# Optimization experiments

Hardware: AMD Instinct MI355X
Metric: run time of the kernel (lower is better)

## Reference

```python
import jax, jax.numpy as jnp
import numpy as np

N_NODES = 100000
N_EDGES = 1600000
IN_DIM = 256
OUT_DIM = 128
EPS = 1e-12  # torch F.normalize default eps


def setup_inputs() -> dict:
    key = jax.random.key(0)
    k1, k2, k3, k4, k5 = jax.random.split(key, 5)
    x = jax.random.normal(k1, (N_NODES, IN_DIM), dtype=jnp.float32)
    edge_index = jax.random.randint(k2, (2, N_EDGES), 0, N_NODES, dtype=jnp.int64)
    # projection (no bias): weight [out, in]
    Wp = jax.random.normal(k3, (OUT_DIM, IN_DIM), dtype=jnp.float32) * 0.05
    # GCNConv internal linear weight [out, out] and output bias [out]
    Wg = jax.random.normal(k4, (OUT_DIM, OUT_DIM), dtype=jnp.float32) * 0.05
    bg = jax.random.normal(k5, (OUT_DIM,), dtype=jnp.float32) * 0.01
    return {"x": x, "edge_index": edge_index, "Wp": Wp, "Wg": Wg, "bg": bg}


def reference(x, edge_index, Wp, Wg, bg):
    n = x.shape[0]
    # projection: x @ Wp^T
    h = x @ Wp.T                      # [N, OUT]
    # GCNConv: transform first, then propagate
    h = h @ Wg.T                      # [N, OUT]
    # add self-loops
    loops = jnp.arange(n, dtype=edge_index.dtype)
    row = jnp.concatenate([edge_index[0], loops])   # source
    col = jnp.concatenate([edge_index[1], loops])   # target
    # symmetric normalization: deg over target index (edge_weight = 1)
    deg = jax.ops.segment_sum(jnp.ones_like(col, dtype=h.dtype), col, num_segments=n)
    dinv = jnp.where(deg > 0, jax.lax.rsqrt(deg), 0.0)
    norm = dinv[row] * dinv[col]                     # [E+N]
    # gather messages from source, scale, scatter-add to target
    msg = h[row] * norm[:, None]                     # [E+N, OUT]
    out = jax.ops.segment_sum(msg, col, num_segments=n)  # [N, OUT]
    out = out + bg
    # F.normalize(dim=1): divide by L2 norm clamped at eps
    nrm = jnp.sqrt(jnp.sum(out * out, axis=1, keepdims=True))
    out = out / jnp.maximum(nrm, EPS)
    return out
```

## Files before the change

kernel.cpp:

```cpp
#include <hip/hip_runtime.h>
#include <hip/hip_fp16.h>

#define NDIM 128
#define KDIM 256
#define MT 5
#define AROW 264
#define CHUNK 6400
#define MAXBUCK 128

typedef _Float16 half8 __attribute__((ext_vector_type(8)));
typedef float float4v __attribute__((ext_vector_type(4)));

__global__ void k_combine_w(const float* __restrict__ Wp, const float* __restrict__ Wg,
                            _Float16* __restrict__ Bfrag) {
    int o = blockIdx.x;
    int i = threadIdx.x;
    float acc = 0.f;
#pragma unroll 4
    for (int k = 0; k < 128; ++k) acc = fmaf(Wg[o * 128 + k], Wp[k * 256 + i], acc);
    int kk = i >> 5, r = i & 31, quad = r >> 3, j = r & 7;
    int ntile = o >> 4, lanen = o & 15, lane = quad * 16 + lanen;
    Bfrag[(((ntile * 8 + kk) * 64) + lane) * 8 + j] = (_Float16)acc;
}

__global__ __launch_bounds__(256) void k_phase1(const int* __restrict__ col, int E,
                                                int* __restrict__ hist, int NBLK, int NBUCK) {
    __shared__ int h[MAXBUCK];
    int tid = threadIdx.x;
    if (tid < MAXBUCK) h[tid] = 0;
    __syncthreads();
    int e0 = blockIdx.x * CHUNK;
    int e1 = min(e0 + CHUNK, E);
    for (int e = e0 + tid; e < e1; e += 256) atomicAdd(&h[col[e] >> 10], 1);
    __syncthreads();
    if (tid < NBUCK) hist[tid * NBLK + blockIdx.x] = h[tid];
}

__global__ __launch_bounds__(1024) void k_scan2(int* __restrict__ hist, int NE) {
    __shared__ int s[1024];
    int t = threadIdx.x;
    int CH = (NE + 1023) >> 10;
    int off = t * CH;
    int sum = 0;
    for (int j = 0; j < CH; ++j) { int idx = off + j; if (idx < NE) sum += hist[idx]; }
    s[t] = sum;
    __syncthreads();
    for (int d = 1; d < 1024; d <<= 1) {
        int y = (t >= d) ? s[t - d] : 0;
        __syncthreads();
        s[t] += y;
        __syncthreads();
    }
    int run = s[t] - sum;
    for (int j = 0; j < CH; ++j) {
        int idx = off + j;
        if (idx < NE) { int v = hist[idx]; hist[idx] = run; run += v; }
    }
}

__global__ __launch_bounds__(256) void k_phase3(const int* __restrict__ ei, int E,
                                                const int* __restrict__ offs, int NBLK, int NBUCK,
                                                int2* __restrict__ tmp) {
    __shared__ int cur[MAXBUCK];
    int tid = threadIdx.x;
    if (tid < NBUCK) cur[tid] = offs[tid * NBLK + blockIdx.x];
    __syncthreads();
    int e0 = blockIdx.x * CHUNK;
    int e1 = min(e0 + CHUNK, E);
    for (int e = e0 + tid; e < e1; e += 256) {
        int r = ei[e];
        int c = ei[E + e];
        int p = atomicAdd(&cur[c >> 10], 1);
        tmp[p] = make_int2(r, c);
    }
}

__global__ __launch_bounds__(1024) void k_fine(const int2* __restrict__ tmp,
                                               const int* __restrict__ offs, int NBLK, int NBUCK,
                                               int N, int E,
                                               int* __restrict__ sortedRow,
                                               int* __restrict__ cnt,
                                               int* __restrict__ rowStart) {
    __shared__ int scnt[1024];
    __shared__ int cur[1024];
    int b = blockIdx.x;
    int t = threadIdx.x;
    int nodeBase = b << 10;
    int start = offs[b * NBLK];
    int end = (b + 1 < NBUCK) ? offs[(b + 1) * NBLK] : E;

    scnt[t] = 0;
    __syncthreads();
    for (int p = start + t; p < end; p += 1024) atomicAdd(&scnt[tmp[p].y - nodeBase], 1);
    __syncthreads();
    int v = scnt[t];
    for (int d = 1; d < 1024; d <<= 1) {
        int y = (t >= d) ? scnt[t - d] : 0;
        __syncthreads();
        scnt[t] += y;
        __syncthreads();
    }
    int excl = scnt[t] - v;
    int node = nodeBase + t;
    if (node < N) {
        cnt[node] = v;
        rowStart[node] = start + excl;
    }
    cur[t] = start + excl;
    __syncthreads();
    for (int p = start + t; p < end; p += 1024) {
        int2 pr = tmp[p];
        int slot = atomicAdd(&cur[pr.y - nodeBase], 1);
        sortedRow[slot] = pr.x;
    }
    if (b == NBUCK - 1 && t == 0) rowStart[N] = E;
}

__global__ __launch_bounds__(256) void k_gemm_mfma(const float* __restrict__ x,
                                                   const _Float16* __restrict__ Bfrag,
                                                   const int* __restrict__ cnt,
                                                   _Float16* __restrict__ g, int nrows) {
    __shared__ __align__(16) _Float16 xs[16 * AROW];
    int tid  = threadIdx.x;
    int lane = tid & 63;
    int w    = tid >> 6;
    int quad = lane >> 4;
    int lcol = lane & 15;

    const half8* Bv = (const half8*)Bfrag;
    half8 b0[8], b1[8];
#pragma unroll
    for (int kk = 0; kk < 8; ++kk) {
        b0[kk] = Bv[(w * 8 + kk) * 64 + lane];
        b1[kk] = Bv[((w + 4) * 8 + kk) * 64 + lane];
    }

    long base = (long)blockIdx.x * (16 * MT);
    for (int t = 0; t < MT; ++t) {
        long m0 = base + t * 16;
        __syncthreads();
        const float4* xv = (const float4*)(x + m0 * KDIM);
#pragma unroll
        for (int ii = 0; ii < 4; ++ii) {
            int idx = tid + ii * 256;
            int m = idx >> 6, k4 = idx & 63;
            float4 v = xv[idx];
            _Float16* d = &xs[m * AROW + k4 * 4];
            d[0] = (_Float16)v.x; d[1] = (_Float16)v.y;
            d[2] = (_Float16)v.z; d[3] = (_Float16)v.w;
        }
        __syncthreads();

        float4v acc0 = {0.f, 0.f, 0.f, 0.f}, acc1 = {0.f, 0.f, 0.f, 0.f};
#pragma unroll
        for (int kk = 0; kk < 8; ++kk) {
            half8 a = *(const half8*)(&xs[lcol * AROW + kk * 32 + quad * 8]);
            acc0 = __builtin_amdgcn_mfma_f32_16x16x32_f16(a, b0[kk], acc0, 0, 0, 0);
            acc1 = __builtin_amdgcn_mfma_f32_16x16x32_f16(a, b1[kk], acc1, 0, 0, 0);
        }

#pragma unroll
        for (int r = 0; r < 4; ++r) {
            long node = m0 + quad * 4 + r;
            float di = rsqrtf((float)(cnt[node] + 1));
            g[node * NDIM + w * 16 + lcol]        = (_Float16)(acc0[r] * di);
            g[node * NDIM + (w + 4) * 16 + lcol]  = (_Float16)(acc1[r] * di);
        }
    }
}

__global__ __launch_bounds__(256) void k_gather(const _Float16* __restrict__ g,
                                                const int* __restrict__ rowStart,
                                                const int* __restrict__ sortedRow,
                                                const int* __restrict__ cnt,
                                                const float* __restrict__ bg,
                                                float* __restrict__ out) {
    int lane = threadIdx.x & 63;
    int i = blockIdx.x * 4 + (threadIdx.x >> 6);
    const int s = rowStart[i];
    const int e = rowStart[i + 1];
    const int g4  = lane >> 4;
    const int r16 = lane & 15;

    const half8* __restrict__ gv = (const half8*)g;

    float acc[8];
#pragma unroll
    for (int j = 0; j < 8; ++j) acc[j] = 0.f;

    int p = s;
    for (; p + 16 <= e; p += 16) {
        int r0 = sortedRow[p + g4];
        int r1 = sortedRow[p + 4 + g4];
        int r2 = sortedRow[p + 8 + g4];
        int r3 = sortedRow[p + 12 + g4];
        half8 v0 = gv[(size_t)r0 * 16 + r16];
        half8 v1 = gv[(size_t)r1 * 16 + r16];
        half8 v2 = gv[(size_t)r2 * 16 + r16];
        half8 v3 = gv[(size_t)r3 * 16 + r16];
#pragma unroll
        for (int j = 0; j < 8; ++j)
            acc[j] += ((float)v0[j] + (float)v1[j]) + ((float)v2[j] + (float)v3[j]);
    }
    for (; p + 4 <= e; p += 4) {
        int r0 = sortedRow[p + g4];
        half8 v0 = gv[(size_t)r0 * 16 + r16];
#pragma unroll
        for (int j = 0; j < 8; ++j) acc[j] += (float)v0[j];
    }
    if (p + g4 < e) {
        int r0 = sortedRow[p + g4];
        half8 v0 = gv[(size_t)r0 * 16 + r16];
#pragma unroll
        for (int j = 0; j < 8; ++j) acc[j] += (float)v0[j];
    }

#pragma unroll
    for (int j = 0; j < 8; ++j) {
        acc[j] += __shfl_xor(acc[j], 16);
        acc[j] += __shfl_xor(acc[j], 32);
    }

    half8 sv = gv[(size_t)i * 16 + r16];
#pragma unroll
    for (int j = 0; j < 8; ++j) acc[j] += (float)sv[j];

    float di = rsqrtf((float)(cnt[i] + 1));
    float4 b0 = ((const float4*)bg)[r16 * 2];
    float4 b1 = ((const float4*)bg)[r16 * 2 + 1];
    float v[8];
    v[0] = fmaf(di, acc[0], b0.x);
    v[1] = fmaf(di, acc[1], b0.y);
    v[2] = fmaf(di, acc[2], b0.z);
    v[3] = fmaf(di, acc[3], b0.w);
    v[4] = fmaf(di, acc[4], b1.x);
    v[5] = fmaf(di, acc[5], b1.y);
    v[6] = fmaf(di, acc[6], b1.z);
    v[7] = fmaf(di, acc[7], b1.w);

    float sq = 0.f;
#pragma unroll
    for (int j = 0; j < 8; ++j) sq += v[j] * v[j];
    sq += __shfl_xor(sq, 1);
    sq += __shfl_xor(sq, 2);
    sq += __shfl_xor(sq, 4);
    sq += __shfl_xor(sq, 8);
    float scale = 1.0f / fmaxf(sqrtf(sq), 1e-12f);

    if (g4 == 0) {
        float4 o0 = make_float4(v[0] * scale, v[1] * scale, v[2] * scale, v[3] * scale);
        float4 o1 = make_float4(v[4] * scale, v[5] * scale, v[6] * scale, v[7] * scale);
        ((float4*)out)[(size_t)i * 32 + r16 * 2]     = o0;
        ((float4*)out)[(size_t)i * 32 + r16 * 2 + 1] = o1;
    }
}

extern "C" void kernel_launch(void* const* d_in, const int* in_sizes, int n_in,
                              void* d_out, int out_size, void* d_ws, size_t ws_size,
                              hipStream_t stream) {
    const float* x  = (const float*)d_in[0];
    const int*   ei = (const int*)  d_in[1];
    const float* Wp = (const float*)d_in[2];
    const float* Wg = (const float*)d_in[3];
    const float* bg = (const float*)d_in[4];
    float* out = (float*)d_out;

    const int N = in_sizes[0] / KDIM;
    const int E = in_sizes[1] / 2;

    const int NBLK  = (E + CHUNK - 1) / CHUNK;
    const int NBUCK = (N + 1023) >> 10;
    const int NE    = NBLK * NBUCK;

    char* p = (char*)d_ws;
    auto carve = [&](size_t bytes) { void* r = (void*)p; p += (bytes + 255) & ~(size_t)255; return r; };
    _Float16* g      = (_Float16*)carve((size_t)N * NDIM * 2);
    int*   sortedRow = (int*)  carve((size_t)E * 4);
    int2*  tmp       = (int2*) carve((size_t)E * 8);
    _Float16* Bfrag  = (_Float16*)carve((size_t)KDIM * NDIM * 2);
    int*   cnt       = (int*)  carve((size_t)N * 4);
    int*   rowStart  = (int*)  carve((size_t)(N + 1) * 4);
    int*   hist      = (int*)  carve((size_t)NE * 4);

    hipLaunchKernelGGL(k_combine_w, dim3(NDIM), dim3(KDIM), 0, stream, Wp, Wg, Bfrag);
    hipLaunchKernelGGL(k_phase1, dim3(NBLK), dim3(256), 0, stream, ei + E, E, hist, NBLK, NBUCK);
    hipLaunchKernelGGL(k_scan2, dim3(1), dim3(1024), 0, stream, hist, NE);
    hipLaunchKernelGGL(k_phase3, dim3(NBLK), dim3(256), 0, stream, ei, E, hist, NBLK, NBUCK, tmp);
    hipLaunchKernelGGL(k_fine, dim3(NBUCK), dim3(1024), 0, stream, tmp, hist, NBLK, NBUCK, N, E,
                       sortedRow, cnt, rowStart);
    hipLaunchKernelGGL(k_gemm_mfma, dim3(N / (16 * MT)), dim3(256), 0, stream, x, Bfrag, cnt, g, N);
    hipLaunchKernelGGL(k_gather, dim3(N / 4), dim3(256), 0, stream,
                       g, rowStart, sortedRow, cnt, bg, out);
}
```

Measured before the change: 353.5 us.

## Replace two-level bucket sort with atomic-count rank plus scan CSR build

Replaces the bucketed two-pass CSR construction (histogram, bucket scatter to a temporary pair array, per-bucket fine sort) with a global atomic count per target node that records each edge's rank, a three-kernel scan, and a direct scatter using rowStart+rank. This removes the 8-byte-per-edge temporary array and the per-bucket shared-memory passes. In exchange it uses global atomics on a 100k-entry counter array, and the within-row edge order is nondeterministic. It also adds a memset and more kernel launches. Ranks are stored as 16-bit values, which assumes no node has more than 65535 incoming edges.

```diff
diff --git a/kernel.cpp b/kernel.cpp
--- a/kernel.cpp
+++ b/kernel.cpp
@@ -5,8 +5,6 @@
 #define KDIM 256
 #define MT 5
 #define AROW 264
-#define CHUNK 6400
-#define MAXBUCK 128
 
 typedef _Float16 half8 __attribute__((ext_vector_type(8)));
 typedef float float4v __attribute__((ext_vector_type(4)));
@@ -23,27 +21,26 @@
     Bfrag[(((ntile * 8 + kk) * 64) + lane) * 8 + j] = (_Float16)acc;
 }
 
-__global__ __launch_bounds__(256) void k_phase1(const int* __restrict__ col, int E,
-                                                int* __restrict__ hist, int NBLK, int NBUCK) {
-    __shared__ int h[MAXBUCK];
-    int tid = threadIdx.x;
-    if (tid < MAXBUCK) h[tid] = 0;
-    __syncthreads();
-    int e0 = blockIdx.x * CHUNK;
-    int e1 = min(e0 + CHUNK, E);
-    for (int e = e0 + tid; e < e1; e += 256) atomicAdd(&h[col[e] >> 10], 1);
-    __syncthreads();
-    if (tid < NBUCK) hist[tid * NBLK + blockIdx.x] = h[tid];
-}
-
-__global__ __launch_bounds__(1024) void k_scan2(int* __restrict__ hist, int NE) {
+__global__ __launch_bounds__(256) void k_count(const int* __restrict__ ei, int E,
+                                               int* __restrict__ cnt,
+                                               unsigned short* __restrict__ rank) {
+    int e = blockIdx.x * 256 + threadIdx.x;
+    int stride = gridDim.x * 256;
+    for (; e < E; e += stride) {
+        int c = ei[E + e];
+        int r = atomicAdd(&cnt[c], 1);
+        rank[e] = (unsigned short)r;
+    }
+}
+
+__global__ __launch_bounds__(1024) void k_scan_blk(const int* __restrict__ cnt, int N,
+                                                   int* __restrict__ rowStart,
+                                                   int* __restrict__ blockSum) {
     __shared__ int s[1024];
     int t = threadIdx.x;
-    int CH = (NE + 1023) >> 10;
-    int off = t * CH;
-    int sum = 0;
-    for (int j = 0; j < CH; ++j) { int idx = off + j; if (idx < NE) sum += hist[idx]; }
-    s[t] = sum;
+    int i = blockIdx.x * 1024 + t;
+    int v = (i < N) ? cnt[i] : 0;
+    s[t] = v;
     __syncthreads();
     for (int d = 1; d < 1024; d <<= 1) {
         int y = (t >= d) ? s[t - d] : 0;
@@ -51,69 +48,43 @@
         s[t] += y;
         __syncthreads();
     }
-    int run = s[t] - sum;
-    for (int j = 0; j < CH; ++j) {
-        int idx = off + j;
-        if (idx < NE) { int v = hist[idx]; hist[idx] = run; run += v; }
-    }
-}
-
-__global__ __launch_bounds__(256) void k_phase3(const int* __restrict__ ei, int E,
-                                                const int* __restrict__ offs, int NBLK, int NBUCK,
-                                                int2* __restrict__ tmp) {
-    __shared__ int cur[MAXBUCK];
-    int tid = threadIdx.x;
-    if (tid < NBUCK) cur[tid] = offs[tid * NBLK + blockIdx.x];
+    if (i < N) rowStart[i] = s[t] - v;
+    if (t == 1023) blockSum[blockIdx.x] = s[t];
+}
+
+__global__ __launch_bounds__(1024) void k_scan_top(int* __restrict__ blockSum, int nb,
+                                                   int* __restrict__ rowStart, int N, int E) {
+    __shared__ int s[1024];
+    int t = threadIdx.x;
+    int v = (t < nb) ? blockSum[t] : 0;
+    s[t] = v;
     __syncthreads();
-    int e0 = blockIdx.x * CHUNK;
-    int e1 = min(e0 + CHUNK, E);
-    for (int e = e0 + tid; e < e1; e += 256) {
-        int r = ei[e];
+    for (int d = 1; d < 1024; d <<= 1) {
+        int y = (t >= d) ? s[t - d] : 0;
+        __syncthreads();
+        s[t] += y;
+        __syncthreads();
+    }
+    if (t < nb) blockSum[t] = s[t] - v;
+    if (t == 0) rowStart[N] = E;
+}
+
+__global__ __launch_bounds__(256) void k_scan_add(int* __restrict__ rowStart,
+                                                  const int* __restrict__ blockOff, int N) {
+    int i = blockIdx.x * 256 + threadIdx.x;
+    if (i < N) rowStart[i] += blockOff[i >> 10];
+}
+
+__global__ __launch_bounds__(256) void k_scatter(const int* __restrict__ ei, int E,
+                                                 const int* __restrict__ rowStart,
+                                                 const unsigned short* __restrict__ rank,
+                                                 int* __restrict__ sortedRow) {
+    int e = blockIdx.x * 256 + threadIdx.x;
+    int stride = gridDim.x * 256;
+    for (; e < E; e += stride) {
         int c = ei[E + e];
-        int p = atomicAdd(&cur[c >> 10], 1);
-        tmp[p] = make_int2(r, c);
-    }
-}
-
-__global__ __launch_bounds__(1024) void k_fine(const int2* __restrict__ tmp,
-                                               const int* __restrict__ offs, int NBLK, int NBUCK,
-                                               int N, int E,
-                                               int* __restrict__ sortedRow,
-                                               int* __restrict__ cnt,
-                                               int* __restrict__ rowStart) {
-    __shared__ int scnt[1024];
-    __shared__ int cur[1024];
-    int b = blockIdx.x;
-    int t = threadIdx.x;
-    int nodeBase = b << 10;
-    int start = offs[b * NBLK];
-    int end = (b + 1 < NBUCK) ? offs[(b + 1) * NBLK] : E;
-
-    scnt[t] = 0;
-    __syncthreads();
-    for (int p = start + t; p < end; p += 1024) atomicAdd(&scnt[tmp[p].y - nodeBase], 1);
-    __syncthreads();
-    int v = scnt[t];
-    for (int d = 1; d < 1024; d <<= 1) {
-        int y = (t >= d) ? scnt[t - d] : 0;
-        __syncthreads();
-        scnt[t] += y;
-        __syncthreads();
-    }
-    int excl = scnt[t] - v;
-    int node = nodeBase + t;
-    if (node < N) {
-        cnt[node] = v;
-        rowStart[node] = start + excl;
-    }
-    cur[t] = start + excl;
-    __syncthreads();
-    for (int p = start + t; p < end; p += 1024) {
-        int2 pr = tmp[p];
-        int slot = atomicAdd(&cur[pr.y - nodeBase], 1);
-        sortedRow[slot] = pr.x;
-    }
-    if (b == NBUCK - 1 && t == 0) rowStart[N] = E;
+        sortedRow[rowStart[c] + (int)rank[e]] = ei[e];
+    }
 }
 
 __global__ __launch_bounds__(256) void k_gemm_mfma(const float* __restrict__ x,
@@ -268,26 +239,26 @@
     const int N = in_sizes[0] / KDIM;
     const int E = in_sizes[1] / 2;
 
-    const int NBLK  = (E + CHUNK - 1) / CHUNK;
     const int NBUCK = (N + 1023) >> 10;
-    const int NE    = NBLK * NBUCK;
 
     char* p = (char*)d_ws;
     auto carve = [&](size_t bytes) { void* r = (void*)p; p += (bytes + 255) & ~(size_t)255; return r; };
     _Float16* g      = (_Float16*)carve((size_t)N * NDIM * 2);
     int*   sortedRow = (int*)  carve((size_t)E * 4);
-    int2*  tmp       = (int2*) carve((size_t)E * 8);
+    unsigned short* rank = (unsigned short*)carve((size_t)E * 2);
     _Float16* Bfrag  = (_Float16*)carve((size_t)KDIM * NDIM * 2);
     int*   cnt       = (int*)  carve((size_t)N * 4);
     int*   rowStart  = (int*)  carve((size_t)(N + 1) * 4);
-    int*   hist      = (int*)  carve((size_t)NE * 4);
+    int*   blockSum  = (int*)  carve((size_t)NBUCK * 4);
+
+    hipMemsetAsync(cnt, 0, (size_t)N * 4, stream);
 
     hipLaunchKernelGGL(k_combine_w, dim3(NDIM), dim3(KDIM), 0, stream, Wp, Wg, Bfrag);
-    hipLaunchKernelGGL(k_phase1, dim3(NBLK), dim3(256), 0, stream, ei + E, E, hist, NBLK, NBUCK);
-    hipLaunchKernelGGL(k_scan2, dim3(1), dim3(1024), 0, stream, hist, NE);
-    hipLaunchKernelGGL(k_phase3, dim3(NBLK), dim3(256), 0, stream, ei, E, hist, NBLK, NBUCK, tmp);
-    hipLaunchKernelGGL(k_fine, dim3(NBUCK), dim3(1024), 0, stream, tmp, hist, NBLK, NBUCK, N, E,
-                       sortedRow, cnt, rowStart);
+    hipLaunchKernelGGL(k_count, dim3(2048), dim3(256), 0, stream, ei, E, cnt, rank);
+    hipLaunchKernelGGL(k_scan_blk, dim3(NBUCK), dim3(1024), 0, stream, cnt, N, rowStart, blockSum);
+    hipLaunchKernelGGL(k_scan_top, dim3(1), dim3(1024), 0, stream, blockSum, NBUCK, rowStart, N, E);
+    hipLaunchKernelGGL(k_scan_add, dim3((N + 255) / 256), dim3(256), 0, stream, rowStart, blockSum, N);
+    hipLaunchKernelGGL(k_scatter, dim3(2048), dim3(256), 0, stream, ei, E, rowStart, rank, sortedRow);
     hipLaunchKernelGGL(k_gemm_mfma, dim3(N / (16 * MT)), dim3(256), 0, stream, x, Bfrag, cnt, g, N);
     hipLaunchKernelGGL(k_gather, dim3(N / 4), dim3(256), 0, stream,
                        g, rowStart, sortedRow, cnt, bg, out);
```

Result: slower. 372.8 us (+5.5%).
